# Kernel tuning notes

Hardware: AMD Instinct MI355X
Metric: run time of the kernel (lower is better)

Reference implementation:

```python
import jax, jax.numpy as jnp
import numpy as np

NUM_SAMPLES = 10  # hardcoded numOfSamples in __computeIntensityIntegral


def setup_inputs() -> dict:
    key = jax.random.key(0)
    ks = jax.random.split(key, 7)
    E = 2_000_000
    N, D = 10_000, 3
    tInit = jax.random.uniform(ks[0], (E,), dtype=jnp.float32) * 100.0
    dur = jax.random.uniform(ks[1], (E,), dtype=jnp.float32) + 0.01
    tLast = tInit + dur
    k = jax.random.randint(ks[2], (E,), 0, 3, dtype=jnp.int32)
    gamma = jax.random.uniform(ks[3], (N, 1), dtype=jnp.float32)
    x0 = jax.random.uniform(ks[4], (N, D), dtype=jnp.float32)
    v0 = jax.random.uniform(ks[5], (N, D), dtype=jnp.float32)
    a0 = jax.random.uniform(ks[6], (N, D), dtype=jnp.float32)
    return {"tInit": tInit, "tLast": tLast, "k": k,
            "gamma": gamma, "x0": x0, "v0": v0, "a0": a0}


def reference(tInit, tLast, k, gamma, x0, v0, a0):
    # Forward always uses the node pair (i=0, j=1).
    dx = x0[0] - x0[1]  # [D]
    dv = v0[0] - v0[1]  # [D]
    da = a0[0] - a0[1]  # [D]
    g = gamma[0, 0] + gamma[1, 0]  # scalar

    step = (tLast - tInit) / NUM_SAMPLES  # [E] (linspace endpoint=False retstep)
    # time samples: tInit + n*step for n in 0..9  -> [E, S]
    t = tInit[:, None] + step[:, None] * jnp.arange(NUM_SAMPLES, dtype=tInit.dtype)
    # relative position at each sample: dx + dv*t + da*t^2/2  -> [E, S, D]
    diff = dx + dv * t[..., None] + 0.5 * da * (t * t)[..., None]
    dist = jnp.sqrt(jnp.sum(diff * diff, axis=-1))  # [E, S]
    lam = jnp.exp(g - dist)  # intensity [E, S]
    ci = jnp.sum(lam, axis=-1) * step  # integral per event [E]

    # neg_logLikelihood = sum(-ci + 1{k>0} * log(ci)); return -neg_logLikelihood
    log_ci = jnp.log(ci)
    nll = jnp.sum(-ci + jnp.where(k > 0, log_ci, 0.0))
    return -nll
```

## Files before the change

### kernel.cpp

```cpp
#include <hip/hip_runtime.h>
#include <hip/hip_bf16.h>


#define NUM_SAMPLES 10

__global__ void init_acc(double* acc) { *acc = 0.0; }

__device__ __forceinline__ double event_term(
    float ti, float tl, int kk,
    float dx0, float dx1, float dx2,
    float dv0, float dv1, float dv2,
    float ha0, float ha1, float ha2,
    float g)
{
    float step = (tl - ti) * (1.0f / NUM_SAMPLES);
    float dist[NUM_SAMPLES];
    float s = 0.0f;
#pragma unroll
    for (int n = 0; n < NUM_SAMPLES; ++n) {
        float t  = fmaf(step, (float)n, ti);
        float t2 = t * t;
        float f0 = fmaf(ha0, t2, fmaf(dv0, t, dx0));
        float f1 = fmaf(ha1, t2, fmaf(dv1, t, dx1));
        float f2 = fmaf(ha2, t2, fmaf(dv2, t, dx2));
        float d2 = fmaf(f0, f0, fmaf(f1, f1, f2 * f2));
        dist[n] = sqrtf(d2);
        s += expf(g - dist[n]);
    }
    float ci = s * step;
    double r = -(double)ci;
    if (kk > 0) {
        float mind = dist[0];
#pragma unroll
        for (int n = 1; n < NUM_SAMPLES; ++n) mind = fminf(mind, dist[n]);
        float se = 0.0f;
#pragma unroll
        for (int n = 0; n < NUM_SAMPLES; ++n) se += expf(mind - dist[n]);
        r += (double)(g - mind) + (double)logf(se) + (double)logf(step);
    }
    return r;
}

__global__ void __launch_bounds__(256)
nhpp_nll_kernel(const float* __restrict__ tInit,
                const float* __restrict__ tLast,
                const int*   __restrict__ k,
                const float* __restrict__ gamma,
                const float* __restrict__ x0,
                const float* __restrict__ v0,
                const float* __restrict__ a0,
                double* __restrict__ acc,
                int E)
{
    const float dx0 = x0[0] - x0[3], dx1 = x0[1] - x0[4], dx2 = x0[2] - x0[5];
    const float dv0 = v0[0] - v0[3], dv1 = v0[1] - v0[4], dv2 = v0[2] - v0[5];
    const float ha0 = 0.5f * (a0[0] - a0[3]);
    const float ha1 = 0.5f * (a0[1] - a0[4]);
    const float ha2 = 0.5f * (a0[2] - a0[5]);
    const float g   = gamma[0] + gamma[1];

    const int nq = (E + 3) >> 2;
    double local = 0.0;

    for (int q = blockIdx.x * blockDim.x + threadIdx.x; q < nq;
         q += gridDim.x * blockDim.x) {
        const int base = q << 2;
        if (base + 3 < E) {
            float4 ti = ((const float4*)tInit)[q];
            float4 tl = ((const float4*)tLast)[q];
            int4   kv = ((const int4*)k)[q];
            local += event_term(ti.x, tl.x, kv.x, dx0,dx1,dx2, dv0,dv1,dv2, ha0,ha1,ha2, g);
            local += event_term(ti.y, tl.y, kv.y, dx0,dx1,dx2, dv0,dv1,dv2, ha0,ha1,ha2, g);
            local += event_term(ti.z, tl.z, kv.z, dx0,dx1,dx2, dv0,dv1,dv2, ha0,ha1,ha2, g);
            local += event_term(ti.w, tl.w, kv.w, dx0,dx1,dx2, dv0,dv1,dv2, ha0,ha1,ha2, g);
        } else {
            for (int e = base; e < E; ++e)
                local += event_term(tInit[e], tLast[e], k[e],
                                    dx0,dx1,dx2, dv0,dv1,dv2, ha0,ha1,ha2, g);
        }
    }

#pragma unroll
    for (int off = 32; off > 0; off >>= 1)
        local += __shfl_down(local, off, 64);

    __shared__ double wsum[4];
    const int lane = threadIdx.x & 63;
    const int wid  = threadIdx.x >> 6;
    if (lane == 0) wsum[wid] = local;
    __syncthreads();
    if (threadIdx.x == 0) {
        double b = wsum[0] + wsum[1] + wsum[2] + wsum[3];
        atomicAdd(acc, b);
    }
}

__global__ void finalize_out(const double* acc, float* out) {
    double v = -acc[0];
    if (!(v == v)) v = 0.0;
    if (v >  3.0e38) v =  3.0e38;
    if (v < -3.0e38) v = -3.0e38;
    out[0] = (float)v;
}

extern "C" void kernel_launch(void* const* d_in, const int* in_sizes, int n_in,
                              void* d_out, int out_size, void* d_ws, size_t ws_size,
                              hipStream_t stream) {
    const float* tInit = (const float*)d_in[0];
    const float* tLast = (const float*)d_in[1];
    const int*   k     = (const int*)d_in[2];
    const float* gamma = (const float*)d_in[3];
    const float* x0    = (const float*)d_in[4];
    const float* v0    = (const float*)d_in[5];
    const float* a0    = (const float*)d_in[6];
    float* out = (float*)d_out;
    double* acc = (double*)d_ws;

    const int E = in_sizes[0];
    const int nq = (E + 3) >> 2;
    const int threads = 256;
    int blocks = (nq + threads - 1) / threads;
    if (blocks > 4096) blocks = 4096;

    init_acc<<<1, 1, 0, stream>>>(acc);
    nhpp_nll_kernel<<<blocks, threads, 0, stream>>>(tInit, tLast, k, gamma,
                                                    x0, v0, a0, acc, E);
    finalize_out<<<1, 1, 0, stream>>>(acc, out);
}
```

Measured before the change: 109.5 us.

## Share one log-sum-exp pass and replace atomics with per-block partial sums

Each event's per-sample intensities now go through a single max-shifted exp pass. That pass yields both the integral and its log, removing the second exp loop for events with k>0. Fast intrinsics (__expf, __logf, builtin sqrt) replace the precise library calls. The global double atomicAdd and init kernel are replaced by per-block partials reduced in a 256-thread finalize kernel, and the grid cap is halved. This lowers arithmetic and launch count at some accuracy cost, since the fast approximations and the rescaled exp may differ slightly from the reference.

```diff
diff --git a/kernel.cpp b/kernel.cpp
--- a/kernel.cpp
+++ b/kernel.cpp
@@ -3,8 +3,6 @@
 
 
 #define NUM_SAMPLES 10
-
-__global__ void init_acc(double* acc) { *acc = 0.0; }
 
 __device__ __forceinline__ double event_term(
     float ti, float tl, int kk,
@@ -13,9 +11,8 @@
     float ha0, float ha1, float ha2,
     float g)
 {
-    float step = (tl - ti) * (1.0f / NUM_SAMPLES);
-    float dist[NUM_SAMPLES];
-    float s = 0.0f;
+    const float step = (tl - ti) * (1.0f / NUM_SAMPLES);
+    float u[NUM_SAMPLES];
 #pragma unroll
     for (int n = 0; n < NUM_SAMPLES; ++n) {
         float t  = fmaf(step, (float)n, ti);
@@ -24,21 +21,19 @@
         float f1 = fmaf(ha1, t2, fmaf(dv1, t, dx1));
         float f2 = fmaf(ha2, t2, fmaf(dv2, t, dx2));
         float d2 = fmaf(f0, f0, fmaf(f1, f1, f2 * f2));
-        dist[n] = sqrtf(d2);
-        s += expf(g - dist[n]);
+        u[n] = g - __builtin_amdgcn_sqrtf(d2);
     }
-    float ci = s * step;
-    double r = -(double)ci;
-    if (kk > 0) {
-        float mind = dist[0];
+    float m = u[0];
 #pragma unroll
-        for (int n = 1; n < NUM_SAMPLES; ++n) mind = fminf(mind, dist[n]);
-        float se = 0.0f;
+    for (int n = 1; n < NUM_SAMPLES; ++n) m = fmaxf(m, u[n]);
+    float S = 0.0f;
 #pragma unroll
-        for (int n = 0; n < NUM_SAMPLES; ++n) se += expf(mind - dist[n]);
-        r += (double)(g - mind) + (double)logf(se) + (double)logf(step);
-    }
-    return r;
+    for (int n = 0; n < NUM_SAMPLES; ++n) S += __expf(u[n] - m);
+
+    const float ci = step * __expf(m) * S;
+    const float log_ci = m + __logf(S) + __logf(step);
+    const float w = (kk > 0) ? 1.0f : 0.0f;
+    return (double)(-ci) + (double)(w * log_ci);
 }
 
 __global__ void __launch_bounds__(256)
@@ -49,7 +44,7 @@
                 const float* __restrict__ x0,
                 const float* __restrict__ v0,
                 const float* __restrict__ a0,
-                double* __restrict__ acc,
+                double* __restrict__ partial,
                 int E)
 {
     const float dx0 = x0[0] - x0[3], dx1 = x0[1] - x0[4], dx2 = x0[2] - x0[5];
@@ -89,18 +84,30 @@
     const int wid  = threadIdx.x >> 6;
     if (lane == 0) wsum[wid] = local;
     __syncthreads();
-    if (threadIdx.x == 0) {
-        double b = wsum[0] + wsum[1] + wsum[2] + wsum[3];
-        atomicAdd(acc, b);
-    }
+    if (threadIdx.x == 0)
+        partial[blockIdx.x] = wsum[0] + wsum[1] + wsum[2] + wsum[3];
 }
 
-__global__ void finalize_out(const double* acc, float* out) {
-    double v = -acc[0];
-    if (!(v == v)) v = 0.0;
-    if (v >  3.0e38) v =  3.0e38;
-    if (v < -3.0e38) v = -3.0e38;
-    out[0] = (float)v;
+__global__ void __launch_bounds__(256)
+finalize_out(const double* __restrict__ partial, int nblocks, float* out) {
+    double local = 0.0;
+    for (int i = threadIdx.x; i < nblocks; i += 256)
+        local += partial[i];
+#pragma unroll
+    for (int off = 32; off > 0; off >>= 1)
+        local += __shfl_down(local, off, 64);
+    __shared__ double wsum[4];
+    const int lane = threadIdx.x & 63;
+    const int wid  = threadIdx.x >> 6;
+    if (lane == 0) wsum[wid] = local;
+    __syncthreads();
+    if (threadIdx.x == 0) {
+        double v = -(wsum[0] + wsum[1] + wsum[2] + wsum[3]);
+        if (!(v == v)) v = 0.0;
+        if (v >  3.0e38) v =  3.0e38;
+        if (v < -3.0e38) v = -3.0e38;
+        out[0] = (float)v;
+    }
 }
 
 extern "C" void kernel_launch(void* const* d_in, const int* in_sizes, int n_in,
@@ -114,16 +121,15 @@
     const float* v0    = (const float*)d_in[5];
     const float* a0    = (const float*)d_in[6];
     float* out = (float*)d_out;
-    double* acc = (double*)d_ws;
+    double* partial = (double*)d_ws;
 
     const int E = in_sizes[0];
     const int nq = (E + 3) >> 2;
     const int threads = 256;
     int blocks = (nq + threads - 1) / threads;
-    if (blocks > 4096) blocks = 4096;
+    if (blocks > 2048) blocks = 2048;
 
-    init_acc<<<1, 1, 0, stream>>>(acc);
     nhpp_nll_kernel<<<blocks, threads, 0, stream>>>(tInit, tLast, k, gamma,
-                                                    x0, v0, a0, acc, E);
-    finalize_out<<<1, 1, 0, stream>>>(acc, out);
+                                                    x0, v0, a0, partial, E);
+    finalize_out<<<1, threads, 0, stream>>>(partial, blocks, out);
 }
```

New measurement: 94.97 us. 1.15x faster.
